# Kernel optimization log

Measured on AMD Instinct MI355X. Metric: run time of the kernel, lower is better.

The kernel has to match this reference:

```python
import jax, jax.numpy as jnp
import numpy as np
import math

CHANNELS = 512
OUT_CHANNELS = 512
N_HEADS = 8
WINDOW = 4
K_CH = CHANNELS // N_HEADS


def _conv1x1(x, W, b):
    # x: (B, C_in, T), W: (C_out, C_in), b: (C_out,)
    return jnp.einsum('oc,bct->bot', W, x) + b[None, :, None]


def _get_relative_embeddings(emb, length, window=WINDOW):
    # emb: (H, 2*window+1, k_ch) -> (H, 2*length-1, k_ch)
    pad_length = max(length - (window + 1), 0)
    start = max(window + 1 - length, 0)
    e = jnp.pad(emb, ((0, 0), (pad_length, pad_length), (0, 0))) if pad_length > 0 else emb
    return e[:, start:start + 2 * length - 1]


def _relative_to_absolute(x):
    # x: (B, H, L, 2L-1) -> (B, H, L, L)
    b, h, L, _ = x.shape
    x = jnp.pad(x, ((0, 0), (0, 0), (0, 0), (0, 1)))          # (B,H,L,2L)
    xf = x.reshape(b, h, L * 2 * L)
    xf = jnp.pad(xf, ((0, 0), (0, 0), (L - 1, 0)))
    return xf.reshape(b, h, L + 1, 2 * L - 1)[:, :, :L, L - 1:]


def _absolute_to_relative(x):
    # x: (B, H, L, L) -> (B, H, L, 2L-1)
    b, h, L, _ = x.shape
    x = jnp.pad(x, ((0, 0), (0, 0), (0, 0), (0, L - 1)))       # (B,H,L,2L-1)
    xf = x.reshape(b, h, L * (2 * L - 1))
    xf = jnp.pad(xf, ((0, 0), (0, 0), (L, 0)))
    return xf.reshape(b, h, L, 2 * L)[:, :, :, 1:]


def setup_inputs() -> dict:
    key = jax.random.key(0)
    ks = jax.random.split(key, 16)
    B, C, T = 4, CHANNELS, 1024
    xavier = math.sqrt(2.0 / (C + C))
    rel_std = K_CH ** -0.5
    return {
        'x_q': jax.random.normal(ks[0], (B, C, T), jnp.float32),
        'x_k': jax.random.normal(ks[1], (B, C, T), jnp.float32),
        'x_v': jax.random.normal(ks[2], (B, C, T), jnp.float32),
        'Wq': jax.random.normal(ks[3], (C, C), jnp.float32) * xavier,
        'bq': jnp.zeros((C,), jnp.float32),
        'Wk': jax.random.normal(ks[4], (C, C), jnp.float32) * xavier,
        'bk': jnp.zeros((C,), jnp.float32),
        'Wv': jax.random.normal(ks[5], (C, C), jnp.float32) * xavier,
        'bv': jnp.zeros((C,), jnp.float32),
        'Wo': jax.random.normal(ks[6], (OUT_CHANNELS, C), jnp.float32) * xavier,
        'bo': jnp.zeros((OUT_CHANNELS,), jnp.float32),
        'emb_rel_k': jax.random.normal(ks[7], (N_HEADS, 2 * WINDOW + 1, K_CH), jnp.float32) * rel_std,
        'emb_rel_v': jax.random.normal(ks[8], (N_HEADS, 2 * WINDOW + 1, K_CH), jnp.float32) * rel_std,
    }


def reference(x_q, x_k, x_v, Wq, bq, Wk, bk, Wv, bv, Wo, bo, emb_rel_k, emb_rel_v):
    q = _conv1x1(x_q, Wq, bq)
    k = _conv1x1(x_k, Wk, bk)
    v = _conv1x1(x_v, Wv, bv)
    B, C, T = q.shape
    # (B, C, T) -> (B, H, T, k_ch); head h owns contiguous k_ch channel chunk
    qh = q.reshape(B, N_HEADS, K_CH, T).transpose(0, 1, 3, 2) / math.sqrt(K_CH)
    kh = k.reshape(B, N_HEADS, K_CH, T).transpose(0, 1, 3, 2)
    vh = v.reshape(B, N_HEADS, K_CH, T).transpose(0, 1, 3, 2)
    scores = jnp.einsum('bhtd,bhsd->bhts', qh, kh)              # (B,H,T,T)
    rel_k = _get_relative_embeddings(emb_rel_k, T)              # (H,2T-1,d)
    rel_logits = jnp.einsum('bhtd,hmd->bhtm', qh, rel_k)        # (B,H,T,2T-1)
    scores = scores + _relative_to_absolute(rel_logits)
    attn = jax.nn.softmax(scores, axis=-1)
    ctx = jnp.einsum('bhts,bhsd->bhtd', attn, vh)
    rel_w = _absolute_to_relative(attn)                         # (B,H,T,2T-1)
    rel_v = _get_relative_embeddings(emb_rel_v, T)
    ctx = ctx + jnp.einsum('bhtm,hmd->bhtd', rel_w, rel_v)
    out = ctx.transpose(0, 1, 3, 2).reshape(B, C, T)
    return _conv1x1(out, Wo, bo)
```

## Files before the change

kernel.cpp:

```cpp
#include <hip/hip_runtime.h>

#define T_LEN 1024
#define NH 8
#define DH 64
#define CCH 512
#define LOG2E 1.44269504088896340736f

typedef _Float16 f16;
typedef _Float16 f16x8 __attribute__((ext_vector_type(8)));
typedef _Float16 f16x4 __attribute__((ext_vector_type(4)));
typedef float f32x4 __attribute__((ext_vector_type(4)));

__device__ __forceinline__ void dma16(const void* g, void* l)
{
    __builtin_amdgcn_global_load_lds((const __attribute__((address_space(1))) void*)g,
                                     (__attribute__((address_space(3))) void*)l, 16, 0, 0);
}

__global__ __launch_bounds__(256)
void prep_kernel(const float* __restrict__ x0, const float* __restrict__ x1,
                 const float* __restrict__ x2, const float* __restrict__ W0,
                 const float* __restrict__ W1, const float* __restrict__ W2,
                 const float* __restrict__ W3, f16* __restrict__ o0,
                 f16* __restrict__ o1, f16* __restrict__ o2, f16* __restrict__ w0,
                 f16* __restrict__ w1, f16* __restrict__ w2, f16* __restrict__ w3,
                 int B)
{
    const int z = blockIdx.z;
    if (z < 3 * B) {
        const int t0 = blockIdx.x * 64, c0 = blockIdx.y * 64;
        const int which = z / B, b = z % B;
        const float* x = (which == 0) ? x0 : (which == 1) ? x1 : x2;
        f16* o = (which == 0) ? o0 : (which == 1) ? o1 : o2;

        __shared__ float L[64 * 68];
        const int cl = threadIdx.x & 63, g = threadIdx.x >> 6;
        const float* src = x + ((size_t)(b * CCH + c0 + cl)) * T_LEN + t0 + g * 16;
        #pragma unroll
        for (int j = 0; j < 4; ++j)
            *(float4*)&L[cl * 68 + g * 16 + 4 * j] = *(const float4*)&src[4 * j];
        __syncthreads();
        const int tl = threadIdx.x & 63, cg = (threadIdx.x >> 6) * 16;
        f16 h[16];
        #pragma unroll
        for (int j = 0; j < 16; ++j) h[j] = (f16)L[(cg + j) * 68 + tl];
        f16* dst = o + ((size_t)(b * T_LEN + t0 + tl)) * CCH + c0 + cg;
        *(f16x8*)&dst[0] = *(f16x8*)&h[0];
        *(f16x8*)&dst[8] = *(f16x8*)&h[8];
    } else {
        const int slice = z - 3 * B;
        size_t i = ((size_t)(slice * 128 + blockIdx.y * 16 + blockIdx.x) * 256 + threadIdx.x) * 4;
        const int wi = (int)(i >> 18);
        const size_t off = i & 262143;
        const float* src = (wi == 0) ? W0 : (wi == 1) ? W1 : (wi == 2) ? W2 : W3;
        f16* dst = (wi == 0) ? w0 : (wi == 1) ? w1 : (wi == 2) ? w2 : w3;
        float4 v4 = *(const float4*)&src[off];
        f16x4 h = {(f16)v4.x, (f16)v4.y, (f16)v4.z, (f16)v4.w};
        *(f16x4*)&dst[off] = h;
    }
}

__global__ __launch_bounds__(256)
void proj_qkv(const f16* __restrict__ xq, const f16* __restrict__ xk,
              const f16* __restrict__ xv, const f16* __restrict__ wq,
              const f16* __restrict__ wk, const f16* __restrict__ wv,
              const float* __restrict__ bq, const float* __restrict__ bk,
              const float* __restrict__ bv, f16* __restrict__ qo,
              f16* __restrict__ ko, f16* __restrict__ vo)
{
    const int which = blockIdx.z;
    const f16* X = (which == 0) ? xq : (which == 1) ? xk : xv;
    const f16* W = (which == 0) ? wq : (which == 1) ? wk : wv;
    const float* bias = (which == 0) ? bq : (which == 1) ? bk : bv;
    const float scale = (which == 0) ? 0.125f * LOG2E : 1.0f;

    const int r0 = blockIdx.x * 64;
    const int o0 = blockIdx.y * 128;
    const int tid = threadIdx.x;
    const int w = tid >> 6, lane = tid & 63;
    const int quad = lane >> 4, l15 = lane & 15;

    __shared__ __align__(16) f16 Xs[64 * 64];
    __shared__ __align__(16) f16 Wsh[128 * 64];

    const int srow = tid >> 3;
    const int scol = ((tid & 7) ^ (srow & 7)) << 3;

    const f16* Xg = X + (size_t)(r0 + srow) * CCH + scol;
    const f16* Wg = W + (size_t)(o0 + srow) * CCH + scol;

    const int ax = (which < 2) ? (w >> 1) : (w & 1);
    const int aw = (which < 2) ? (w & 1) : (w >> 1);

    f32x4 acc[8] = {};

    for (int kc = 0; kc < 8; ++kc) {
        if (kc) __syncthreads();
        const int c1 = kc * 64;
        #pragma unroll
        for (int jj = 0; jj < 4; ++jj)
            dma16(Wg + c1 + (size_t)(32 * jj) * CCH, &Wsh[((size_t)tid + 256 * jj) * 8]);
        #pragma unroll
        for (int jj = 0; jj < 2; ++jj)
            dma16(Xg + c1 + (size_t)(32 * jj) * CCH, &Xs[((size_t)tid + 256 * jj) * 8]);
        __syncthreads();

        #pragma unroll
        for (int ks = 0; ks < 2; ++ks) {
            const int sl = ((ks * 4 + quad) ^ (l15 & 7)) << 3;
            f16x8 xf[2], wf[4];
            #pragma unroll
            for (int i = 0; i < 2; ++i)
                xf[i] = *(const f16x8*)&Xs[(32 * ax + 16 * i + l15) * 64 + sl];
            #pragma unroll
            for (int j = 0; j < 4; ++j)
                wf[j] = *(const f16x8*)&Wsh[(64 * aw + 16 * j + l15) * 64 + sl];
            if (which < 2) {
                #pragma unroll
                for (int i = 0; i < 2; ++i)
                    #pragma unroll
                    for (int j = 0; j < 4; ++j)
                        acc[i * 4 + j] = __builtin_amdgcn_mfma_f32_16x16x32_f16(
                            xf[i], wf[j], acc[i * 4 + j], 0, 0, 0);
            } else {
                #pragma unroll
                for (int i = 0; i < 4; ++i)
                    #pragma unroll
                    for (int j = 0; j < 2; ++j)
                        acc[i * 2 + j] = __builtin_amdgcn_mfma_f32_16x16x32_f16(
                            wf[i], xf[j], acc[i * 2 + j], 0, 0, 0);
            }
        }
    }

    if (which < 2) {
        f16* out = (which == 0) ? qo : ko;
        float bl[4];
        #pragma unroll
        for (int j = 0; j < 4; ++j) bl[j] = bias[o0 + 64 * aw + 16 * j + l15];
        #pragma unroll
        for (int i = 0; i < 2; ++i)
            #pragma unroll
            for (int r = 0; r < 4; ++r) {
                size_t row = (size_t)(r0 + 32 * ax + 16 * i + 4 * quad + r) * CCH;
                #pragma unroll
                for (int j = 0; j < 4; ++j)
                    out[row + o0 + 64 * aw + 16 * j + l15] =
                        (f16)((acc[i * 4 + j][r] + bl[j]) * scale);
            }
    } else {
        const int bb = r0 >> 10, tb = r0 & 1023;
        #pragma unroll
        for (int i = 0; i < 4; ++i) {
            float4 bv4 = *(const float4*)&bias[o0 + 64 * aw + 16 * i + 4 * quad];
            float bl[4] = {bv4.x, bv4.y, bv4.z, bv4.w};
            #pragma unroll
            for (int r = 0; r < 4; ++r) {
                size_t row = ((size_t)(bb * CCH + o0 + 64 * aw + 16 * i + 4 * quad + r)) * T_LEN;
                #pragma unroll
                for (int j = 0; j < 2; ++j)
                    vo[row + tb + 32 * ax + 16 * j + l15] =
                        (f16)(acc[i * 2 + j][r] + bl[r]);
            }
        }
    }
}

__global__ __launch_bounds__(512, 4)
void attn_mfma(const f16* __restrict__ q, const f16* __restrict__ kk,
               const f16* __restrict__ v, const float* __restrict__ ekg,
               const float* __restrict__ evg, f16* __restrict__ ctx)
{
    const int t0 = blockIdx.x * 64, h = blockIdx.y, b = blockIdx.z;
    const int tid = threadIdx.x;
    const int w = tid >> 6, lane = tid & 63;
    const int quad = lane >> 4, l15 = lane & 15;
    const int qw = w & 3, sw = w >> 2;

    __shared__ __align__(16) f16 Qs[4096], Ps[4096];
    __shared__ __align__(16) f16 KV[2][2][4096];
    __shared__ float eks[576], evs[576];
    __shared__ float lsp[2][64];

    const int srow = tid >> 3;
    const int scol = ((tid & 7) ^ (srow & 7)) << 3;

    for (int i = tid; i < 576; i += 512) {
        eks[i] = ekg[h * 576 + i];
        evs[i] = evg[h * 576 + i];
    }

    const f16* gk = kk + ((size_t)(b * T_LEN + srow)) * CCH + h * DH + scol;
    const f16* gv = v + ((size_t)(b * CCH + h * DH + srow)) * T_LEN + scol;

    dma16(q + ((size_t)(b * T_LEN + t0 + srow)) * CCH + h * DH + scol, &Qs[(size_t)tid * 8]);
    dma16(gk, &KV[0][0][(size_t)tid * 8]);
    dma16(gv, &KV[0][1][(size_t)tid * 8]);
    __syncthreads();

    f16x8 qf[2];
    #pragma unroll
    for (int ks = 0; ks < 2; ++ks)
        qf[ks] = *(const f16x8*)&Qs[(16 * qw + l15) * 64 + (((ks * 4 + quad) ^ (l15 & 7)) << 3)];

    const int myt = 16 * qw + l15;
    float Ssum = 0.f;
    f32x4 O[4] = {};

    const bool corner_hi = (blockIdx.x == 0);
    const bool corner_lo = (blockIdx.x == 15);

    for (int it = 0; it < 16; ++it) {
        const int kb = it, cb = it & 1;
        if (it) __syncthreads();

        if (it < 15) {
            const int nb = cb ^ 1;
            dma16(gk + (size_t)((it + 1) * 64) * CCH, &KV[nb][0][(size_t)tid * 8]);
            dma16(gv + (it + 1) * 64, &KV[nb][1][(size_t)tid * 8]);
        }

        f32x4 S[2] = {};
        __builtin_amdgcn_s_setprio(1);
        #pragma unroll
        for (int ks = 0; ks < 2; ++ks) {
            #pragma unroll
            for (int cti = 0; cti < 2; ++cti) {
                const int ct = 2 * sw + cti;
                f16x8 aa = *(const f16x8*)&KV[cb][0][(16 * ct + l15) * 64 +
                                                     (((ks * 4 + quad) ^ (l15 & 7)) << 3)];
                S[cti] = __builtin_amdgcn_mfma_f32_16x16x32_f16(aa, qf[ks], S[cti], 0, 0, 0);
            }
        }
        __builtin_amdgcn_s_setprio(0);

        if ((corner_hi && kb == 15) || (corner_lo && kb == 0)) {
            const int s0g = kb * 64;
            #pragma unroll
            for (int cti = 0; cti < 2; ++cti) {
                const int ct = 2 * sw + cti;
                #pragma unroll
                for (int r = 0; r < 4; ++r) {
                    int t_g = t0 + myt;
                    int s_g = s0g + 16 * ct + 4 * quad + r;
                    int df = s_g - t_g;
                    if (df >= 1019 && df <= 1023) {
                        const float* ekp = &eks[(df - 1019) * 64];
                        float sacc = 0.f;
                        for (int d = 0; d < 64; ++d)
                            sacc += (float)Qs[myt * 64 + (((d >> 3) ^ (myt & 7)) << 3) + (d & 7)] * ekp[d];
                        S[cti][r] += sacc;
                    } else if (df >= -1023 && df <= -1021) {
                        const float* ekp = &eks[(1029 + df) * 64];
                        const int t2 = myt - 1;
                        float sacc = 0.f;
                        for (int d = 0; d < 64; ++d)
                            sacc += (float)Qs[t2 * 64 + (((d >> 3) ^ (t2 & 7)) << 3) + (d & 7)] * ekp[d];
                        S[cti][r] += sacc;
                    }
                }
            }
        }

        #pragma unroll
        for (int cti = 0; cti < 2; ++cti) {
            const int ct = 2 * sw + cti;
            f16x4 pk_;
            #pragma unroll
            for (int r = 0; r < 4; ++r) {
                float p = exp2f(S[cti][r]);
                Ssum += p;
                pk_[r] = (f16)p;
            }
            int colh = (((2 * ct + (quad >> 1)) ^ (myt & 7)) << 3) + (quad & 1) * 4;
            *(f16x4*)&Ps[myt * 64 + colh] = pk_;
        }

        __builtin_amdgcn_s_setprio(1);
        {
            f16x8 aa = *(const f16x8*)&Ps[(16 * qw + l15) * 64 +
                                          (((sw * 4 + quad) ^ (l15 & 7)) << 3)];
            #pragma unroll
            for (int ct = 0; ct < 4; ++ct) {
                f16x8 bf = *(const f16x8*)&KV[cb][1][(16 * ct + l15) * 64 +
                                                     (((sw * 4 + quad) ^ (l15 & 7)) << 3)];
                O[ct] = __builtin_amdgcn_mfma_f32_16x16x32_f16(aa, bf, O[ct], 0, 0, 0);
            }
        }
        __builtin_amdgcn_s_setprio(0);

        const int s0g = kb * 64;
        if (s0g <= t0 + 67 && s0g + 63 >= t0 - 4) {
            #pragma unroll
            for (int r = 0; r < 4; ++r) {
                int t_loc = 16 * qw + 4 * quad + r;
                int t_g = t0 + t_loc;
                int slo = max(max(s0g, t_g - 4), s0g + 32 * sw);
                int shi = min(min(s0g + 63, t_g + 4), s0g + 32 * sw + 31);
                for (int s = slo; s <= shi; ++s) {
                    int sl = s - s0g;
                    float p = (float)Ps[t_loc * 64 + (((sl >> 3) ^ (t_loc & 7)) << 3) + (sl & 7)];
                    const float* evp = &evs[(s - t_g + 4) * 64];
                    #pragma unroll
                    for (int ct = 0; ct < 4; ++ct)
                        O[ct][r] += p * evp[16 * ct + l15];
                }
            }
        }
    }

    Ssum += __shfl_xor(Ssum, 16);
    Ssum += __shfl_xor(Ssum, 32);
    if (quad == 0) lsp[sw][myt] = Ssum;
    __syncthreads();

    float* Ored = (float*)&KV[0][0][0];
    if (sw == 1) {
        #pragma unroll
        for (int r = 0; r < 4; ++r) {
            const int t_loc = 16 * qw + 4 * quad + r;
            #pragma unroll
            for (int ct = 0; ct < 4; ++ct)
                Ored[t_loc * 66 + 16 * ct + l15] = O[ct][r];
        }
    }
    __syncthreads();

    if (sw == 0) {
        #pragma unroll
        for (int r = 0; r < 4; ++r) {
            const int t_loc = 16 * qw + 4 * quad + r;
            const float rl = 1.0f / (lsp[0][t_loc] + lsp[1][t_loc]);
            size_t rowo = ((size_t)(b * T_LEN + t0 + t_loc)) * CCH + h * DH;
            #pragma unroll
            for (int ct = 0; ct < 4; ++ct)
                ctx[rowo + 16 * ct + l15] =
                    (f16)((O[ct][r] + Ored[t_loc * 66 + 16 * ct + l15]) * rl);
        }
    }
}

__global__ __launch_bounds__(256)
void proj_out(const f16* __restrict__ ctx, const f16* __restrict__ Wo,
              const float* __restrict__ bo, float* __restrict__ out)
{
    const int r0 = blockIdx.x * 64;
    const int o0 = blockIdx.y * 64;
    const int tid = threadIdx.x;
    const int w = tid >> 6, lane = tid & 63;
    const int quad = lane >> 4, l15 = lane & 15;
    const int a  = w >> 1;
    const int b2 = w & 1;

    __shared__ __align__(16) f16 Cs[64 * 64];
    __shared__ __align__(16) f16 Wsh[64 * 64];

    const int srow = tid >> 3;
    const int scol = ((tid & 7) ^ (srow & 7)) << 3;

    const f16* Cg = ctx + (size_t)(r0 + srow) * CCH + scol;
    const f16* Wg = Wo + (size_t)(o0 + srow) * CCH + scol;

    f32x4 acc[2][2] = {};

    for (int kc = 0; kc < 8; ++kc) {
        if (kc) __syncthreads();
        const int c1 = kc * 64;
        #pragma unroll
        for (int jj = 0; jj < 2; ++jj) {
            dma16(Wg + c1 + (size_t)(32 * jj) * CCH, &Wsh[((size_t)tid + 256 * jj) * 8]);
            dma16(Cg + c1 + (size_t)(32 * jj) * CCH, &Cs[((size_t)tid + 256 * jj) * 8]);
        }
        __syncthreads();

        #pragma unroll
        for (int ks = 0; ks < 2; ++ks) {
            const int sl = ((ks * 4 + quad) ^ (l15 & 7)) << 3;
            f16x8 wf[2], cf[2];
            #pragma unroll
            for (int i = 0; i < 2; ++i)
                wf[i] = *(const f16x8*)&Wsh[(32 * a + 16 * i + l15) * 64 + sl];
            #pragma unroll
            for (int j = 0; j < 2; ++j)
                cf[j] = *(const f16x8*)&Cs[(32 * b2 + 16 * j + l15) * 64 + sl];
            #pragma unroll
            for (int i = 0; i < 2; ++i)
                #pragma unroll
                for (int j = 0; j < 2; ++j)
                    acc[i][j] = __builtin_amdgcn_mfma_f32_16x16x32_f16(
                        wf[i], cf[j], acc[i][j], 0, 0, 0);
        }
    }

    const int bb = r0 >> 10, tb = r0 & 1023;
    #pragma unroll
    for (int i = 0; i < 2; ++i) {
        float4 bv4 = *(const float4*)&bo[o0 + 32 * a + 16 * i + 4 * quad];
        float bl[4] = {bv4.x, bv4.y, bv4.z, bv4.w};
        #pragma unroll
        for (int r = 0; r < 4; ++r) {
            size_t row = ((size_t)(bb * CCH + o0 + 32 * a + 16 * i + 4 * quad + r)) * T_LEN;
            #pragma unroll
            for (int j = 0; j < 2; ++j)
                out[row + tb + 32 * b2 + 16 * j + l15] = acc[i][j][r] + bl[r];
        }
    }
}

extern "C" void kernel_launch(void* const* d_in, const int* in_sizes, int n_in,
                              void* d_out, int out_size, void* d_ws, size_t ws_size,
                              hipStream_t stream)
{
    const float* x_q = (const float*)d_in[0];
    const float* x_k = (const float*)d_in[1];
    const float* x_v = (const float*)d_in[2];
    const float* Wq  = (const float*)d_in[3];
    const float* bq  = (const float*)d_in[4];
    const float* Wk  = (const float*)d_in[5];
    const float* bk  = (const float*)d_in[6];
    const float* Wv  = (const float*)d_in[7];
    const float* bv  = (const float*)d_in[8];
    const float* Wo  = (const float*)d_in[9];
    const float* bo  = (const float*)d_in[10];
    const float* erk = (const float*)d_in[11];
    const float* erv = (const float*)d_in[12];

    const int B = in_sizes[0] / (CCH * T_LEN);
    const size_t te = (size_t)B * CCH * T_LEN;
    const size_t we = (size_t)CCH * CCH;

    f16* p = (f16*)d_ws;
    f16* xTq = p; p += te;
    f16* xTk = p; p += te;
    f16* xTv = p; p += te;
    f16* wqh = p; p += we;
    f16* wkh = p; p += we;
    f16* wvh = p; p += we;
    f16* woh = p; p += we;
    f16* qh  = p; p += te;
    f16* kh  = p; p += te;
    f16* vh  = p; p += te;
    f16* ch  = p; p += te;

    dim3 blk(256);
    prep_kernel<<<dim3(16, 8, 3 * B + 8), blk, 0, stream>>>(
        x_q, x_k, x_v, Wq, Wk, Wv, Wo, xTq, xTk, xTv, wqh, wkh, wvh, woh, B);
    proj_qkv<<<dim3(B * 16, 4, 3), blk, 0, stream>>>(
        xTq, xTk, xTv, wqh, wkh, wvh, bq, bk, bv, qh, kh, vh);
    attn_mfma<<<dim3(T_LEN / 64, NH, B), dim3(512), 0, stream>>>(
        qh, kh, vh, erk, erv, ch);
    proj_out<<<dim3(B * 16, 8), blk, 0, stream>>>(
        ch, woh, bo, (float*)d_out);
}
```

Baseline: 145.6 us.

## Load K/V fragments directly into registers and widen GEMM K-chunks to 128

The attention kernel drops the double-buffered LDS staging of K and V tiles. Each wave now loads its MFMA operand fragments straight from global memory into registers, with a 2x unrolled loop, which removes the per-iteration barriers and the LDS traffic. The QKV projection and output projection kernels double the K-chunk per stage from 64 to 128 with a 16-way XOR swizzle, halving the number of sync/load rounds but using more LDS. The risk is exposed global-load latency in attention, since there is no explicit prefetch and each block re-reads K/V with less coalesced 16-byte accesses.

```diff
diff --git a/kernel.cpp b/kernel.cpp
--- a/kernel.cpp
+++ b/kernel.cpp
@@ -80,11 +80,11 @@
     const int w = tid >> 6, lane = tid & 63;
     const int quad = lane >> 4, l15 = lane & 15;
 
-    __shared__ __align__(16) f16 Xs[64 * 64];
-    __shared__ __align__(16) f16 Wsh[128 * 64];
-
-    const int srow = tid >> 3;
-    const int scol = ((tid & 7) ^ (srow & 7)) << 3;
+    __shared__ __align__(16) f16 Xs[64 * 128];
+    __shared__ __align__(16) f16 Wsh[128 * 128];
+
+    const int srow = tid >> 4;
+    const int scol = ((tid & 15) ^ srow) << 3;
 
     const f16* Xg = X + (size_t)(r0 + srow) * CCH + scol;
     const f16* Wg = W + (size_t)(o0 + srow) * CCH + scol;
@@ -94,27 +94,27 @@
 
     f32x4 acc[8] = {};
 
-    for (int kc = 0; kc < 8; ++kc) {
+    for (int kc = 0; kc < 4; ++kc) {
         if (kc) __syncthreads();
-        const int c1 = kc * 64;
+        const int c1 = kc * 128;
+        #pragma unroll
+        for (int jj = 0; jj < 8; ++jj)
+            dma16(Wg + c1 + (size_t)(16 * jj) * CCH, &Wsh[((size_t)tid + 256 * jj) * 8]);
         #pragma unroll
         for (int jj = 0; jj < 4; ++jj)
-            dma16(Wg + c1 + (size_t)(32 * jj) * CCH, &Wsh[((size_t)tid + 256 * jj) * 8]);
-        #pragma unroll
-        for (int jj = 0; jj < 2; ++jj)
-            dma16(Xg + c1 + (size_t)(32 * jj) * CCH, &Xs[((size_t)tid + 256 * jj) * 8]);
+            dma16(Xg + c1 + (size_t)(16 * jj) * CCH, &Xs[((size_t)tid + 256 * jj) * 8]);
         __syncthreads();
 
         #pragma unroll
-        for (int ks = 0; ks < 2; ++ks) {
-            const int sl = ((ks * 4 + quad) ^ (l15 & 7)) << 3;
+        for (int ks = 0; ks < 4; ++ks) {
+            const int sl = ((ks * 4 + quad) ^ l15) << 3;
             f16x8 xf[2], wf[4];
             #pragma unroll
             for (int i = 0; i < 2; ++i)
-                xf[i] = *(const f16x8*)&Xs[(32 * ax + 16 * i + l15) * 64 + sl];
+                xf[i] = *(const f16x8*)&Xs[(32 * ax + 16 * i + l15) * 128 + sl];
             #pragma unroll
             for (int j = 0; j < 4; ++j)
-                wf[j] = *(const f16x8*)&Wsh[(64 * aw + 16 * j + l15) * 64 + sl];
+                wf[j] = *(const f16x8*)&Wsh[(64 * aw + 16 * j + l15) * 128 + sl];
             if (which < 2) {
                 #pragma unroll
                 for (int i = 0; i < 2; ++i)
@@ -178,7 +178,7 @@
     const int qw = w & 3, sw = w >> 2;
 
     __shared__ __align__(16) f16 Qs[4096], Ps[4096];
-    __shared__ __align__(16) f16 KV[2][2][4096];
+    __shared__ float Ored[64 * 68];
     __shared__ float eks[576], evs[576];
     __shared__ float lsp[2][64];
 
@@ -190,12 +190,7 @@
         evs[i] = evg[h * 576 + i];
     }
 
-    const f16* gk = kk + ((size_t)(b * T_LEN + srow)) * CCH + h * DH + scol;
-    const f16* gv = v + ((size_t)(b * CCH + h * DH + srow)) * T_LEN + scol;
-
     dma16(q + ((size_t)(b * T_LEN + t0 + srow)) * CCH + h * DH + scol, &Qs[(size_t)tid * 8]);
-    dma16(gk, &KV[0][0][(size_t)tid * 8]);
-    dma16(gv, &KV[0][1][(size_t)tid * 8]);
     __syncthreads();
 
     f16x8 qf[2];
@@ -203,6 +198,9 @@
     for (int ks = 0; ks < 2; ++ks)
         qf[ks] = *(const f16x8*)&Qs[(16 * qw + l15) * 64 + (((ks * 4 + quad) ^ (l15 & 7)) << 3)];
 
+    const f16* Kp = kk + ((size_t)(b * T_LEN + 32 * sw + l15)) * CCH + h * DH + 8 * quad;
+    const f16* Vp = v + ((size_t)(b * CCH + h * DH + l15)) * T_LEN + 32 * sw + 8 * quad;
+
     const int myt = 16 * qw + l15;
     float Ssum = 0.f;
     f32x4 O[4] = {};
@@ -210,32 +208,31 @@
     const bool corner_hi = (blockIdx.x == 0);
     const bool corner_lo = (blockIdx.x == 15);
 
+    #pragma unroll 2
     for (int it = 0; it < 16; ++it) {
-        const int kb = it, cb = it & 1;
-        if (it) __syncthreads();
-
-        if (it < 15) {
-            const int nb = cb ^ 1;
-            dma16(gk + (size_t)((it + 1) * 64) * CCH, &KV[nb][0][(size_t)tid * 8]);
-            dma16(gv + (it + 1) * 64, &KV[nb][1][(size_t)tid * 8]);
-        }
+        const int kb = it;
+        const int s0g = it * 64;
+
+        f16x8 kf[2][2], vf[4];
+        #pragma unroll
+        for (int cti = 0; cti < 2; ++cti)
+            #pragma unroll
+            for (int ks = 0; ks < 2; ++ks)
+                kf[cti][ks] = *(const f16x8*)(Kp + (size_t)(s0g + 16 * cti) * CCH + 32 * ks);
+        #pragma unroll
+        for (int ct = 0; ct < 4; ++ct)
+            vf[ct] = *(const f16x8*)(Vp + (size_t)(16 * ct) * T_LEN + s0g);
 
         f32x4 S[2] = {};
         __builtin_amdgcn_s_setprio(1);
         #pragma unroll
-        for (int ks = 0; ks < 2; ++ks) {
-            #pragma unroll
-            for (int cti = 0; cti < 2; ++cti) {
-                const int ct = 2 * sw + cti;
-                f16x8 aa = *(const f16x8*)&KV[cb][0][(16 * ct + l15) * 64 +
-                                                     (((ks * 4 + quad) ^ (l15 & 7)) << 3)];
-                S[cti] = __builtin_amdgcn_mfma_f32_16x16x32_f16(aa, qf[ks], S[cti], 0, 0, 0);
-            }
-        }
+        for (int ks = 0; ks < 2; ++ks)
+            #pragma unroll
+            for (int cti = 0; cti < 2; ++cti)
+                S[cti] = __builtin_amdgcn_mfma_f32_16x16x32_f16(kf[cti][ks], qf[ks], S[cti], 0, 0, 0);
         __builtin_amdgcn_s_setprio(0);
 
         if ((corner_hi && kb == 15) || (corner_lo && kb == 0)) {
-            const int s0g = kb * 64;
             #pragma unroll
             for (int cti = 0; cti < 2; ++cti) {
                 const int ct = 2 * sw + cti;
@@ -281,15 +278,11 @@
             f16x8 aa = *(const f16x8*)&Ps[(16 * qw + l15) * 64 +
                                           (((sw * 4 + quad) ^ (l15 & 7)) << 3)];
             #pragma unroll
-            for (int ct = 0; ct < 4; ++ct) {
-                f16x8 bf = *(const f16x8*)&KV[cb][1][(16 * ct + l15) * 64 +
-                                                     (((sw * 4 + quad) ^ (l15 & 7)) << 3)];
-                O[ct] = __builtin_amdgcn_mfma_f32_16x16x32_f16(aa, bf, O[ct], 0, 0, 0);
-            }
+            for (int ct = 0; ct < 4; ++ct)
+                O[ct] = __builtin_amdgcn_mfma_f32_16x16x32_f16(aa, vf[ct], O[ct], 0, 0, 0);
         }
         __builtin_amdgcn_s_setprio(0);
 
-        const int s0g = kb * 64;
         if (s0g <= t0 + 67 && s0g + 63 >= t0 - 4) {
             #pragma unroll
             for (int r = 0; r < 4; ++r) {
@@ -314,14 +307,13 @@
     if (quad == 0) lsp[sw][myt] = Ssum;
     __syncthreads();
 
-    float* Ored = (float*)&KV[0][0][0];
     if (sw == 1) {
         #pragma unroll
         for (int r = 0; r < 4; ++r) {
             const int t_loc = 16 * qw + 4 * quad + r;
             #pragma unroll
             for (int ct = 0; ct < 4; ++ct)
-                Ored[t_loc * 66 + 16 * ct + l15] = O[ct][r];
+                Ored[t_loc * 68 + 16 * ct + l15] = O[ct][r];
         }
     }
     __syncthreads();
@@ -335,7 +327,7 @@
             #pragma unroll
             for (int ct = 0; ct < 4; ++ct)
                 ctx[rowo + 16 * ct + l15] =
-                    (f16)((O[ct][r] + Ored[t_loc * 66 + 16 * ct + l15]) * rl);
+                    (f16)((O[ct][r] + Ored[t_loc * 68 + 16 * ct + l15]) * rl);
         }
     }
 }
@@ -352,37 +344,37 @@
     const int a  = w >> 1;
     const int b2 = w & 1;
 
-    __shared__ __align__(16) f16 Cs[64 * 64];
-    __shared__ __align__(16) f16 Wsh[64 * 64];
-
-    const int srow = tid >> 3;
-    const int scol = ((tid & 7) ^ (srow & 7)) << 3;
+    __shared__ __align__(16) f16 Cs[64 * 128];
+    __shared__ __align__(16) f16 Wsh[64 * 128];
+
+    const int srow = tid >> 4;
+    const int scol = ((tid & 15) ^ srow) << 3;
 
     const f16* Cg = ctx + (size_t)(r0 + srow) * CCH + scol;
     const f16* Wg = Wo + (size_t)(o0 + srow) * CCH + scol;
 
     f32x4 acc[2][2] = {};
 
-    for (int kc = 0; kc < 8; ++kc) {
+    for (int kc = 0; kc < 4; ++kc) {
         if (kc) __syncthreads();
-        const int c1 = kc * 64;
-        #pragma unroll
-        for (int jj = 0; jj < 2; ++jj) {
-            dma16(Wg + c1 + (size_t)(32 * jj) * CCH, &Wsh[((size_t)tid + 256 * jj) * 8]);
-            dma16(Cg + c1 + (size_t)(32 * jj) * CCH, &Cs[((size_t)tid + 256 * jj) * 8]);
+        const int c1 = kc * 128;
+        #pragma unroll
+        for (int jj = 0; jj < 4; ++jj) {
+            dma16(Wg + c1 + (size_t)(16 * jj) * CCH, &Wsh[((size_t)tid + 256 * jj) * 8]);
+            dma16(Cg + c1 + (size_t)(16 * jj) * CCH, &Cs[((size_t)tid + 256 * jj) * 8]);
         }
         __syncthreads();
 
         #pragma unroll
-        for (int ks = 0; ks < 2; ++ks) {
-            const int sl = ((ks * 4 + quad) ^ (l15 & 7)) << 3;
+        for (int ks = 0; ks < 4; ++ks) {
+            const int sl = ((ks * 4 + quad) ^ l15) << 3;
             f16x8 wf[2], cf[2];
             #pragma unroll
             for (int i = 0; i < 2; ++i)
-                wf[i] = *(const f16x8*)&Wsh[(32 * a + 16 * i + l15) * 64 + sl];
+                wf[i] = *(const f16x8*)&Wsh[(32 * a + 16 * i + l15) * 128 + sl];
             #pragma unroll
             for (int j = 0; j < 2; ++j)
-                cf[j] = *(const f16x8*)&Cs[(32 * b2 + 16 * j + l15) * 64 + sl];
+                cf[j] = *(const f16x8*)&Cs[(32 * b2 + 16 * j + l15) * 128 + sl];
             #pragma unroll
             for (int i = 0; i < 2; ++i)
                 #pragma unroll
```

New measurement: 225.1 us. 1.55x slower.
